# Kernel optimization log

Hardware: AMD Instinct MI355X
Metric: run time of the kernel (lower is better)

## Reference

```python
import jax, jax.numpy as jnp
import numpy as np

N = 100000
E = 1600000
HID = 128
NODE_DIM = 128


def _sage_conv(h, src, dst, W_l, b_l, W_r, n_nodes):
    # PyG SAGEConv (mean aggr): out = lin_l(mean_{j in N(i)} h_j) + lin_r(h_i)
    msg = h[src]                                            # [E, d] gather
    s = jax.ops.segment_sum(msg, dst, num_segments=n_nodes)  # [N, d]
    cnt = jax.ops.segment_sum(jnp.ones((msg.shape[0], 1), h.dtype), dst,
                              num_segments=n_nodes)          # [N, 1]
    agg = jnp.where(cnt > 0, s / jnp.maximum(cnt, 1.0), 0.0)
    return agg @ W_l + b_l + h @ W_r


def setup_inputs() -> dict:
    key = jax.random.key(0)
    ks = jax.random.split(key, 12)
    sc = 0.05
    return {
        "pos": jax.random.normal(ks[0], (N, 3), jnp.float32),
        "atomic_number": jax.random.randint(ks[1], (N,), 0, 10, jnp.int64)
            if jax.config.jax_enable_x64 else jax.random.randint(ks[1], (N,), 0, 10, jnp.int32),
        "edge_index": jax.random.randint(ks[2], (2, E), 0, N, jnp.int32),
        # input_proj: Linear(4, HID) — stored as [in, out]
        "W_in": jax.random.normal(ks[3], (4, HID), jnp.float32) * sc,
        "b_in": jnp.zeros((HID,), jnp.float32),
        # conv1: SAGEConv(HID, HID): lin_l (bias), lin_r (no bias)
        "W1_l": jax.random.normal(ks[4], (HID, HID), jnp.float32) * sc,
        "b1": jnp.zeros((HID,), jnp.float32),
        "W1_r": jax.random.normal(ks[5], (HID, HID), jnp.float32) * sc,
        # conv2
        "W2_l": jax.random.normal(ks[6], (HID, HID), jnp.float32) * sc,
        "b2": jnp.zeros((HID,), jnp.float32),
        "W2_r": jax.random.normal(ks[7], (HID, HID), jnp.float32) * sc,
        # out: Linear(HID, NODE_DIM)
        "W_out": jax.random.normal(ks[8], (HID, NODE_DIM), jnp.float32) * sc,
        "b_out": jnp.zeros((NODE_DIM,), jnp.float32),
    }


def reference(pos, atomic_number, edge_index, W_in, b_in, W1_l, b1, W1_r,
              W2_l, b2, W2_r, W_out, b_out):
    src, dst = edge_index[0], edge_index[1]
    z_atom = (atomic_number.astype(pos.dtype) / 10.0)[:, None]   # [N, 1]
    x = jnp.concatenate([z_atom, pos], axis=-1)                   # [N, 4]
    h = jax.nn.relu(x @ W_in + b_in)
    h = jax.nn.relu(_sage_conv(h, src, dst, W1_l, b1, W1_r, h.shape[0]))
    h = jax.nn.relu(_sage_conv(h, src, dst, W2_l, b2, W2_r, h.shape[0]))
    node_states = h @ W_out + b_out                               # [N, node_dim]
    return node_states.mean(axis=0), node_states
```

## Files before the change

kernel.cpp:

```cpp
#include <hip/hip_runtime.h>

#define HID 128
#define BK_SHIFT 9
#define BK_NODES 512
#define BKCAP 10240
#define EDGES_PER_BLKA 8192

typedef _Float16 half_t;
typedef __attribute__((ext_vector_type(8))) _Float16 half8;
typedef __attribute__((ext_vector_type(4))) _Float16 half4;
typedef __attribute__((ext_vector_type(4))) float f32x4;

__global__ __launch_bounds__(256) void k_setup(const float* __restrict__ pos,
                                               const int* __restrict__ an,
                                               const float* __restrict__ Win,
                                               const float* __restrict__ bin,
                                               half_t* __restrict__ h0,
                                               const float* __restrict__ w0,
                                               const float* __restrict__ w1,
                                               const float* __restrict__ w2,
                                               const float* __restrict__ w3,
                                               const float* __restrict__ w4,
                                               half_t* __restrict__ o0,
                                               half_t* __restrict__ o1,
                                               half_t* __restrict__ o2,
                                               half_t* __restrict__ o3,
                                               half_t* __restrict__ o4,
                                               int* __restrict__ bcur,
                                               float* __restrict__ outmean,
                                               half_t* __restrict__ h0z,
                                               half_t* __restrict__ h1z,
                                               int n, int gEmbed) {
  int bid = blockIdx.x;
  if (bid < gEmbed) {
    int t = bid * 256 + threadIdx.x;
    int i = t >> 5, cg = t & 31;
    if (i >= n) return;
    int j0 = cg << 2;
    float z  = (float)an[i] / 10.0f;
    float px = pos[3 * i + 0], py = pos[3 * i + 1], pz = pos[3 * i + 2];
    float4 ww0 = *(const float4*)&Win[0 * HID + j0];
    float4 ww1 = *(const float4*)&Win[1 * HID + j0];
    float4 ww2 = *(const float4*)&Win[2 * HID + j0];
    float4 ww3 = *(const float4*)&Win[3 * HID + j0];
    float4 b   = *(const float4*)&bin[j0];
    float4 o;
    o.x = fmaxf(fmaf(z, ww0.x, fmaf(px, ww1.x, fmaf(py, ww2.x, fmaf(pz, ww3.x, b.x)))), 0.f);
    o.y = fmaxf(fmaf(z, ww0.y, fmaf(px, ww1.y, fmaf(py, ww2.y, fmaf(pz, ww3.y, b.y)))), 0.f);
    o.z = fmaxf(fmaf(z, ww0.z, fmaf(px, ww1.z, fmaf(py, ww2.z, fmaf(pz, ww3.z, b.z)))), 0.f);
    o.w = fmaxf(fmaf(z, ww0.w, fmaf(px, ww1.w, fmaf(py, ww2.w, fmaf(pz, ww3.w, b.w)))), 0.f);
    half4 ph;
    ph.x = (half_t)o.x; ph.y = (half_t)o.y; ph.z = (half_t)o.z; ph.w = (half_t)o.w;
    *(half4*)&h0[(size_t)i * HID + j0] = ph;
  } else if (bid < gEmbed + 40) {
    int pb = bid - gEmbed;
    int m = pb >> 3;
    const float* W = (m == 0) ? w0 : (m == 1) ? w1 : (m == 2) ? w2 : (m == 3) ? w3 : w4;
    half_t* out = (m == 0) ? o0 : (m == 1) ? o1 : (m == 2) ? o2 : (m == 3) ? o3 : o4;
    int tid = (pb & 7) * 256 + threadIdx.x;
    int lane = tid & 63;
    int frag = tid >> 6;
    int ks = frag >> 3, nt = frag & 7;
    int k0 = ks * 32 + ((lane >> 4) << 3);
    int col = nt * 16 + (lane & 15);
    half8 v;
#pragma unroll
    for (int i = 0; i < 8; ++i) v[i] = (half_t)W[(k0 + i) * HID + col];
    *(half8*)&out[(size_t)tid * 8] = v;
  } else {
    int i = threadIdx.x;
    bcur[i] = i * BKCAP;
    if (i < HID) outmean[i] = 0.f;
    if (i < HID) h0z[i] = (half_t)0.f;
    else         h1z[i - HID] = (half_t)0.f;
  }
}

__global__ __launch_bounds__(1024) void k_bucketA(const int* __restrict__ src,
                                                  const int* __restrict__ dst,
                                                  int* __restrict__ bcur,
                                                  unsigned* __restrict__ ebuf,
                                                  int e) {
  __shared__ int hist[256];
  __shared__ int resv[256];
  int t = threadIdx.x;
  if (t < 256) hist[t] = 0;
  __syncthreads();
  int e0 = blockIdx.x * EDGES_PER_BLKA;
  int myb[8], myr[8];
  unsigned mypk[8];
#pragma unroll
  for (int i = 0; i < 8; ++i) {
    int idx = e0 + i * 1024 + t;
    if (idx < e) {
      int d = dst[idx];
      int s = src[idx];
      int b = d >> BK_SHIFT;
      myb[i] = b;
      myr[i] = atomicAdd(&hist[b], 1);
      mypk[i] = ((unsigned)s << BK_SHIFT) | (unsigned)(d & (BK_NODES - 1));
    } else {
      myb[i] = -1;
    }
  }
  __syncthreads();
  if (t < 256) resv[t] = (hist[t] > 0) ? atomicAdd(&bcur[t], hist[t]) : 0;
  __syncthreads();
#pragma unroll
  for (int i = 0; i < 8; ++i) {
    if (myb[i] >= 0) ebuf[resv[myb[i]] + myr[i]] = mypk[i];
  }
}

__global__ __launch_bounds__(512) void k_bucketB(const unsigned* __restrict__ ebuf,
                                                 const int* __restrict__ bkend,
                                                 int* __restrict__ offs,
                                                 int* __restrict__ offsE,
                                                 int* __restrict__ csr, int n) {
  __shared__ int hist[BK_NODES];
  __shared__ int red[BK_NODES];
  int b = blockIdx.x;
  int n0 = b << BK_SHIFT;
  int t = threadIdx.x;
  int ebeg = b * BKCAP, eend = bkend[b];
  hist[t] = 0;
  __syncthreads();
  for (int idx = ebeg + t; idx < eend; idx += 512) {
    atomicAdd(&hist[ebuf[idx] & (BK_NODES - 1)], 1);
  }
  __syncthreads();
  int h0 = hist[t];
  red[t] = h0;
  __syncthreads();
  for (int d = 1; d < 512; d <<= 1) {
    int u = (t >= d) ? red[t - d] : 0;
    __syncthreads();
    red[t] += u;
    __syncthreads();
  }
  int base0 = ebeg + (red[t] - h0);
  int g = n0 + t;
  if (g < n) { offs[g] = base0; offsE[g] = base0 + h0; }
  __syncthreads();
  hist[t] = base0;
  __syncthreads();
  for (int idx = ebeg + t; idx < eend; idx += 512) {
    unsigned pk = ebuf[idx];
    int dl = pk & (BK_NODES - 1);
    int slot = atomicAdd(&hist[dl], 1);
    csr[slot] = (int)(pk >> BK_SHIFT);
  }
}

__global__ __launch_bounds__(256) void k_aggmean_f16(const half_t* __restrict__ h,
                                                     const int* __restrict__ csr,
                                                     const int* __restrict__ offs,
                                                     const int* __restrict__ offsE,
                                                     half_t* __restrict__ out, int n) {
  int w = (blockIdx.x * 256 + threadIdx.x) >> 6;
  int lane = threadIdx.x & 63;
  if (w >= n) return;
  int cs = lane & 15, es = lane >> 4;
  int beg = offs[w], end = offsE[w];
  size_t coff = (size_t)(cs * 8);
  float acc[8];
#pragma unroll
  for (int j = 0; j < 8; ++j) acc[j] = 0.f;
  int e = beg;
  for (; e + 16 <= end; e += 16) {
    int s0 = csr[e + es];
    int s1 = csr[e + 4 + es];
    int s2 = csr[e + 8 + es];
    int s3 = csr[e + 12 + es];
    half8 v0 = *(const half8*)&h[(size_t)s0 * HID + coff];
    half8 v1 = *(const half8*)&h[(size_t)s1 * HID + coff];
    half8 v2 = *(const half8*)&h[(size_t)s2 * HID + coff];
    half8 v3 = *(const half8*)&h[(size_t)s3 * HID + coff];
#pragma unroll
    for (int j = 0; j < 8; ++j)
      acc[j] += ((float)v0[j] + (float)v1[j]) + ((float)v2[j] + (float)v3[j]);
  }
  for (; e < end; e += 4) {
    int ee = e + es;
    if (ee < end) {
      int s = csr[ee];
      half8 v = *(const half8*)&h[(size_t)s * HID + coff];
#pragma unroll
      for (int j = 0; j < 8; ++j) acc[j] += (float)v[j];
    }
  }
#pragma unroll
  for (int j = 0; j < 8; ++j) {
    acc[j] += __shfl_xor(acc[j], 16, 64);
    acc[j] += __shfl_xor(acc[j], 32, 64);
  }
  if (es == 0) {
    int c = end - beg;
    float inv = (c > 0) ? 1.0f / (float)c : 0.0f;
    half8 o;
#pragma unroll
    for (int j = 0; j < 8; ++j) o[j] = (half_t)(acc[j] * inv);
    *(half8*)&out[(size_t)w * HID + coff] = o;
  }
}

__global__ __launch_bounds__(256) void k_sage_mfma(const half_t* __restrict__ ha,
                                                   const half_t* __restrict__ hs,
                                                   const half_t* __restrict__ wl,
                                                   const half_t* __restrict__ wr,
                                                   const float* __restrict__ bias,
                                                   half_t* __restrict__ out, int n) {
  int lane = threadIdx.x & 63;
  int wid = threadIdx.x >> 6;
  int row0 = blockIdx.x * 64 + wid * 16;
  if (row0 >= n) return;
  int arow = row0 + (lane & 15);
  int arowc = arow < n ? arow : n - 1;
  size_t abase = (size_t)arowc * HID + ((lane >> 4) << 3);
  const half8* WL = (const half8*)wl;
  const half8* WR = (const half8*)wr;
  f32x4 acc[8];
#pragma unroll
  for (int t = 0; t < 8; ++t) acc[t] = (f32x4){0.f, 0.f, 0.f, 0.f};
#pragma unroll
  for (int ks = 0; ks < 4; ++ks) {
    half8 aD = *(const half8*)&ha[abase + ks * 32];
    half8 aH = *(const half8*)&hs[abase + ks * 32];
    int fb = ks * 8;
#pragma unroll
    for (int nt = 0; nt < 8; ++nt) {
      half8 bl = WL[(size_t)(fb + nt) * 64 + lane];
      half8 br = WR[(size_t)(fb + nt) * 64 + lane];
      acc[nt] = __builtin_amdgcn_mfma_f32_16x16x32_f16(aD, bl, acc[nt], 0, 0, 0);
      acc[nt] = __builtin_amdgcn_mfma_f32_16x16x32_f16(aH, br, acc[nt], 0, 0, 0);
    }
  }
  int rbase = row0 + ((lane >> 4) << 2);
  int cl = lane & 15;
#pragma unroll
  for (int nt = 0; nt < 8; ++nt) {
    int col = nt * 16 + cl;
    float bv = bias[col];
#pragma unroll
    for (int r = 0; r < 4; ++r) {
      int row = rbase + r;
      if (row < n) {
        float v = fmaxf(acc[nt][r] + bv, 0.f);
        out[(size_t)row * HID + col] = (half_t)v;
      }
    }
  }
}

__global__ __launch_bounds__(256) void k_single_mfma(const half_t* __restrict__ hs,
                                                     const half_t* __restrict__ w,
                                                     const float* __restrict__ bias,
                                                     float* __restrict__ out,
                                                     float* __restrict__ part, int n) {
  __shared__ float colsum[HID];
  int tid = threadIdx.x;
  int lane = tid & 63;
  int wid = tid >> 6;
  if (tid < HID) colsum[tid] = 0.f;
  __syncthreads();
  int row0 = blockIdx.x * 64 + wid * 16;
  bool active = row0 < n;
  f32x4 acc[8];
#pragma unroll
  for (int t = 0; t < 8; ++t) acc[t] = (f32x4){0.f, 0.f, 0.f, 0.f};
  if (active) {
    int arow = row0 + (lane & 15);
    int arowc = arow < n ? arow : n - 1;
    size_t abase = (size_t)arowc * HID + ((lane >> 4) << 3);
    const half8* W8 = (const half8*)w;
#pragma unroll
    for (int ks = 0; ks < 4; ++ks) {
      half8 aH = *(const half8*)&hs[abase + ks * 32];
      int fb = ks * 8;
#pragma unroll
      for (int nt = 0; nt < 8; ++nt) {
        half8 b = W8[(size_t)(fb + nt) * 64 + lane];
        acc[nt] = __builtin_amdgcn_mfma_f32_16x16x32_f16(aH, b, acc[nt], 0, 0, 0);
      }
    }
    int rbase = row0 + ((lane >> 4) << 2);
    int cl = lane & 15;
#pragma unroll
    for (int nt = 0; nt < 8; ++nt) {
      int col = nt * 16 + cl;
      float bv = bias[col];
      float csum = 0.f;
#pragma unroll
      for (int r = 0; r < 4; ++r) {
        int row = rbase + r;
        if (row < n) {
          float v = acc[nt][r] + bv;
          out[(size_t)row * HID + col] = v;
          csum += v;
        }
      }
      atomicAdd(&colsum[col], csum);
    }
  }
  __syncthreads();
  if (tid < HID) part[(size_t)blockIdx.x * HID + tid] = colsum[tid];
}

__global__ __launch_bounds__(256) void k_colfinal(const float* __restrict__ part,
                                                  float* __restrict__ outmean,
                                                  int rows, float inv) {
  __shared__ float red[256];
  int t = threadIdx.x;
  int col = t & 127, half = t >> 7;
  int r0 = blockIdx.x * 256;
  float s = 0.f;
  for (int r = half; r < 256; r += 2) {
    int row = r0 + r;
    if (row < rows) s += part[(size_t)row * HID + col];
  }
  red[t] = s;
  __syncthreads();
  if (t < 128) atomicAdd(&outmean[col], (red[t] + red[t + 128]) * inv);
}

extern "C" void kernel_launch(void* const* d_in, const int* in_sizes, int n_in,
                              void* d_out, int out_size, void* d_ws, size_t ws_size,
                              hipStream_t stream) {
  const float* pos  = (const float*)d_in[0];
  const int*   an   = (const int*)d_in[1];
  const int*   ei   = (const int*)d_in[2];
  const float* Win  = (const float*)d_in[3];
  const float* bin  = (const float*)d_in[4];
  const float* W1l  = (const float*)d_in[5];
  const float* b1   = (const float*)d_in[6];
  const float* W1r  = (const float*)d_in[7];
  const float* W2l  = (const float*)d_in[8];
  const float* b2   = (const float*)d_in[9];
  const float* W2r  = (const float*)d_in[10];
  const float* Wout = (const float*)d_in[11];
  const float* bout = (const float*)d_in[12];

  int N = in_sizes[0] / 3;
  int E = in_sizes[2] / 2;
  const int* srcl = ei;
  const int* dstl = ei + E;

  float* outmean = (float*)d_out;
  float* ns      = (float*)d_out + HID;

  char* p = (char*)d_ws;
  auto take = [&](size_t bytes) {
    char* q = p;
    p += (bytes + 255) & ~(size_t)255;
    return q;
  };
  int nbuck = (N + BK_NODES - 1) / BK_NODES;
  half_t*   H0      = (half_t*)take((size_t)(N + 1) * HID * 2);
  half_t*   H1      = (half_t*)take((size_t)(N + 1) * HID * 2);
  half_t*   H2      = (half_t*)take((size_t)N * HID * 2);
  half_t*   D       = (half_t*)take((size_t)N * HID * 2);
  int*      offs    = (int*)take((size_t)N * 4);
  int*      offsE   = (int*)take((size_t)N * 4);
  int*      csr     = (int*)take((size_t)nbuck * BKCAP * 4);
  unsigned* ebuf    = (unsigned*)take((size_t)nbuck * BKCAP * 4);
  int*      bcur    = (int*)take((size_t)256 * 4);
  half_t*   pW1l    = (half_t*)take((size_t)16384 * 2);
  half_t*   pW1r    = (half_t*)take((size_t)16384 * 2);
  half_t*   pW2l    = (half_t*)take((size_t)16384 * 2);
  half_t*   pW2r    = (half_t*)take((size_t)16384 * 2);
  half_t*   pWout   = (half_t*)take((size_t)16384 * 2);
  int gSage = (N + 63) / 64;
  float*    colpart = (float*)take((size_t)gSage * HID * 4);

  int gEmbed = (int)(((size_t)N * 32 + 255) / 256);
  int gWave  = (N + 3) / 4;
  int gBktA  = (E + EDGES_PER_BLKA - 1) / EDGES_PER_BLKA;

  k_setup<<<gEmbed + 41, 256, 0, stream>>>(pos, an, Win, bin, H0,
                                           W1l, W1r, W2l, W2r, Wout,
                                           pW1l, pW1r, pW2l, pW2r, pWout,
                                           bcur, outmean,
                                           &H0[(size_t)N * HID], &H1[(size_t)N * HID],
                                           N, gEmbed);
  k_bucketA<<<gBktA, 1024, 0, stream>>>(srcl, dstl, bcur, ebuf, E);
  k_bucketB<<<nbuck, 512, 0, stream>>>(ebuf, bcur, offs, offsE, csr, N);

  k_aggmean_f16<<<gWave, 256, 0, stream>>>(H0, csr, offs, offsE, D, N);
  k_sage_mfma<<<gSage, 256, 0, stream>>>(D, H0, pW1l, pW1r, b1, H1, N);
  k_aggmean_f16<<<gWave, 256, 0, stream>>>(H1, csr, offs, offsE, D, N);
  k_sage_mfma<<<gSage, 256, 0, stream>>>(D, H1, pW2l, pW2r, b2, H2, N);
  k_single_mfma<<<gSage, 256, 0, stream>>>(H2, pWout, bout, ns, colpart, N);
  k_colfinal<<<(gSage + 255) / 256, 256, 0, stream>>>(colpart, outmean, gSage, 1.0f / (float)N);
}
```

Baseline: 294.5 us.

## Fuse second SAGE layer with output projection and vectorize bucketing loads

Merges the second SAGEConv GEMM with the output linear layer and column-sum into one kernel. The intermediate ReLU activations stay in shared memory instead of going through a global H2 buffer, which removes a kernel launch and a write-then-read of the N×128 fp16 tensor. It also switches the edge bucketing kernels to int4/uint4 vector loads, with each thread handling contiguous edges. That change alters the coalescing pattern and the order of atomics within a bucket, so the CSR neighbor order is no longer the same.

```diff
diff --git a/kernel.cpp b/kernel.cpp
--- a/kernel.cpp
+++ b/kernel.cpp
@@ -86,21 +86,37 @@
   int t = threadIdx.x;
   if (t < 256) hist[t] = 0;
   __syncthreads();
-  int e0 = blockIdx.x * EDGES_PER_BLKA;
+  int base = blockIdx.x * EDGES_PER_BLKA + t * 8;
   int myb[8], myr[8];
   unsigned mypk[8];
-#pragma unroll
-  for (int i = 0; i < 8; ++i) {
-    int idx = e0 + i * 1024 + t;
-    if (idx < e) {
-      int d = dst[idx];
-      int s = src[idx];
-      int b = d >> BK_SHIFT;
+  if (base + 8 <= e) {
+    int4 sa = *(const int4*)&src[base];
+    int4 sb = *(const int4*)&src[base + 4];
+    int4 da = *(const int4*)&dst[base];
+    int4 db = *(const int4*)&dst[base + 4];
+    int ss[8] = {sa.x, sa.y, sa.z, sa.w, sb.x, sb.y, sb.z, sb.w};
+    int dd[8] = {da.x, da.y, da.z, da.w, db.x, db.y, db.z, db.w};
+#pragma unroll
+    for (int i = 0; i < 8; ++i) {
+      int b = dd[i] >> BK_SHIFT;
       myb[i] = b;
       myr[i] = atomicAdd(&hist[b], 1);
-      mypk[i] = ((unsigned)s << BK_SHIFT) | (unsigned)(d & (BK_NODES - 1));
-    } else {
-      myb[i] = -1;
+      mypk[i] = ((unsigned)ss[i] << BK_SHIFT) | (unsigned)(dd[i] & (BK_NODES - 1));
+    }
+  } else {
+#pragma unroll
+    for (int i = 0; i < 8; ++i) {
+      int idx = base + i;
+      if (idx < e) {
+        int d = dst[idx];
+        int s = src[idx];
+        int b = d >> BK_SHIFT;
+        myb[i] = b;
+        myr[i] = atomicAdd(&hist[b], 1);
+        mypk[i] = ((unsigned)s << BK_SHIFT) | (unsigned)(d & (BK_NODES - 1));
+      } else {
+        myb[i] = -1;
+      }
     }
   }
   __syncthreads();
@@ -125,8 +141,19 @@
   int ebeg = b * BKCAP, eend = bkend[b];
   hist[t] = 0;
   __syncthreads();
-  for (int idx = ebeg + t; idx < eend; idx += 512) {
-    atomicAdd(&hist[ebuf[idx] & (BK_NODES - 1)], 1);
+  for (int idx = ebeg + t * 4; idx < eend; idx += 2048) {
+    if (idx + 4 <= eend) {
+      uint4 pk = *(const uint4*)&ebuf[idx];
+      atomicAdd(&hist[pk.x & (BK_NODES - 1)], 1);
+      atomicAdd(&hist[pk.y & (BK_NODES - 1)], 1);
+      atomicAdd(&hist[pk.z & (BK_NODES - 1)], 1);
+      atomicAdd(&hist[pk.w & (BK_NODES - 1)], 1);
+    } else {
+      for (int k = 0; k < 4; ++k) {
+        int id2 = idx + k;
+        if (id2 < eend) atomicAdd(&hist[ebuf[id2] & (BK_NODES - 1)], 1);
+      }
+    }
   }
   __syncthreads();
   int h0 = hist[t];
@@ -144,11 +171,22 @@
   __syncthreads();
   hist[t] = base0;
   __syncthreads();
-  for (int idx = ebeg + t; idx < eend; idx += 512) {
-    unsigned pk = ebuf[idx];
-    int dl = pk & (BK_NODES - 1);
-    int slot = atomicAdd(&hist[dl], 1);
-    csr[slot] = (int)(pk >> BK_SHIFT);
+  for (int idx = ebeg + t * 4; idx < eend; idx += 2048) {
+    if (idx + 4 <= eend) {
+      uint4 pk = *(const uint4*)&ebuf[idx];
+      csr[atomicAdd(&hist[pk.x & (BK_NODES - 1)], 1)] = (int)(pk.x >> BK_SHIFT);
+      csr[atomicAdd(&hist[pk.y & (BK_NODES - 1)], 1)] = (int)(pk.y >> BK_SHIFT);
+      csr[atomicAdd(&hist[pk.z & (BK_NODES - 1)], 1)] = (int)(pk.z >> BK_SHIFT);
+      csr[atomicAdd(&hist[pk.w & (BK_NODES - 1)], 1)] = (int)(pk.w >> BK_SHIFT);
+    } else {
+      for (int k = 0; k < 4; ++k) {
+        int id2 = idx + k;
+        if (id2 < eend) {
+          unsigned pk = ebuf[id2];
+          csr[atomicAdd(&hist[pk & (BK_NODES - 1)], 1)] = (int)(pk >> BK_SHIFT);
+        }
+      }
+    }
   }
 }
 
@@ -252,35 +290,76 @@
   }
 }
 
-__global__ __launch_bounds__(256) void k_single_mfma(const half_t* __restrict__ hs,
-                                                     const half_t* __restrict__ w,
-                                                     const float* __restrict__ bias,
-                                                     float* __restrict__ out,
-                                                     float* __restrict__ part, int n) {
+__global__ __launch_bounds__(256) void k_sage_out(const half_t* __restrict__ ha,
+                                                  const half_t* __restrict__ hs,
+                                                  const half_t* __restrict__ wl,
+                                                  const half_t* __restrict__ wr,
+                                                  const float* __restrict__ bias2,
+                                                  const half_t* __restrict__ wout,
+                                                  const float* __restrict__ bout,
+                                                  float* __restrict__ out,
+                                                  float* __restrict__ part, int n) {
+  __shared__ half_t Hs[64][132];
   __shared__ float colsum[HID];
   int tid = threadIdx.x;
   int lane = tid & 63;
   int wid = tid >> 6;
   if (tid < HID) colsum[tid] = 0.f;
-  __syncthreads();
   int row0 = blockIdx.x * 64 + wid * 16;
   bool active = row0 < n;
-  f32x4 acc[8];
-#pragma unroll
-  for (int t = 0; t < 8; ++t) acc[t] = (f32x4){0.f, 0.f, 0.f, 0.f};
+
   if (active) {
     int arow = row0 + (lane & 15);
     int arowc = arow < n ? arow : n - 1;
     size_t abase = (size_t)arowc * HID + ((lane >> 4) << 3);
-    const half8* W8 = (const half8*)w;
+    const half8* WL = (const half8*)wl;
+    const half8* WR = (const half8*)wr;
+    f32x4 acc[8];
+#pragma unroll
+    for (int t = 0; t < 8; ++t) acc[t] = (f32x4){0.f, 0.f, 0.f, 0.f};
 #pragma unroll
     for (int ks = 0; ks < 4; ++ks) {
+      half8 aD = *(const half8*)&ha[abase + ks * 32];
       half8 aH = *(const half8*)&hs[abase + ks * 32];
       int fb = ks * 8;
 #pragma unroll
       for (int nt = 0; nt < 8; ++nt) {
+        half8 bl = WL[(size_t)(fb + nt) * 64 + lane];
+        half8 br = WR[(size_t)(fb + nt) * 64 + lane];
+        acc[nt] = __builtin_amdgcn_mfma_f32_16x16x32_f16(aD, bl, acc[nt], 0, 0, 0);
+        acc[nt] = __builtin_amdgcn_mfma_f32_16x16x32_f16(aH, br, acc[nt], 0, 0, 0);
+      }
+    }
+    int rb = (lane >> 4) << 2;
+    int cl = lane & 15;
+#pragma unroll
+    for (int nt = 0; nt < 8; ++nt) {
+      int col = nt * 16 + cl;
+      float bv = bias2[col];
+#pragma unroll
+      for (int r = 0; r < 4; ++r) {
+        float v = fmaxf(acc[nt][r] + bv, 0.f);
+        Hs[wid * 16 + rb + r][col] = (half_t)v;
+      }
+    }
+  }
+  __syncthreads();
+
+  if (active) {
+    int lrow = wid * 16 + (lane & 15);
+    int koff = (lane >> 4) << 3;
+    const half8* W8 = (const half8*)wout;
+    f32x4 acc2[8];
+#pragma unroll
+    for (int t = 0; t < 8; ++t) acc2[t] = (f32x4){0.f, 0.f, 0.f, 0.f};
+#pragma unroll
+    for (int ks = 0; ks < 4; ++ks) {
+      half8 aH = *(const half8*)&Hs[lrow][ks * 32 + koff];
+      int fb = ks * 8;
+#pragma unroll
+      for (int nt = 0; nt < 8; ++nt) {
         half8 b = W8[(size_t)(fb + nt) * 64 + lane];
-        acc[nt] = __builtin_amdgcn_mfma_f32_16x16x32_f16(aH, b, acc[nt], 0, 0, 0);
+        acc2[nt] = __builtin_amdgcn_mfma_f32_16x16x32_f16(aH, b, acc2[nt], 0, 0, 0);
       }
     }
     int rbase = row0 + ((lane >> 4) << 2);
@@ -288,13 +367,13 @@
 #pragma unroll
     for (int nt = 0; nt < 8; ++nt) {
       int col = nt * 16 + cl;
-      float bv = bias[col];
+      float bv = bout[col];
       float csum = 0.f;
 #pragma unroll
       for (int r = 0; r < 4; ++r) {
         int row = rbase + r;
         if (row < n) {
-          float v = acc[nt][r] + bv;
+          float v = acc2[nt][r] + bv;
           out[(size_t)row * HID + col] = v;
           csum += v;
         }
@@ -357,7 +436,6 @@
   int nbuck = (N + BK_NODES - 1) / BK_NODES;
   half_t*   H0      = (half_t*)take((size_t)(N + 1) * HID * 2);
   half_t*   H1      = (half_t*)take((size_t)(N + 1) * HID * 2);
-  half_t*   H2      = (half_t*)take((size_t)N * HID * 2);
   half_t*   D       = (half_t*)take((size_t)N * HID * 2);
   int*      offs    = (int*)take((size_t)N * 4);
   int*      offsE   = (int*)take((size_t)N * 4);
@@ -388,7 +466,6 @@
   k_aggmean_f16<<<gWave, 256, 0, stream>>>(H0, csr, offs, offsE, D, N);
   k_sage_mfma<<<gSage, 256, 0, stream>>>(D, H0, pW1l, pW1r, b1, H1, N);
   k_aggmean_f16<<<gWave, 256, 0, stream>>>(H1, csr, offs, offsE, D, N);
-  k_sage_mfma<<<gSage, 256, 0, stream>>>(D, H1, pW2l, pW2r, b2, H2, N);
-  k_single_mfma<<<gSage, 256, 0, stream>>>(H2, pWout, bout, ns, colpart, N);
+  k_sage_out<<<gSage, 256, 0, stream>>>(D, H1, pW2l, pW2r, b2, pWout, bout, ns, colpart, N);
   k_colfinal<<<(gSage + 255) / 256, 256, 0, stream>>>(colpart, outmean, gSage, 1.0f / (float)N);
 }
```

After: 278.3 us, median of 2. 1.06x faster.
